# Kernel tuning notes

Hardware: AMD Instinct MI355X
Metric: run time of the kernel (lower is better)

The kernel has to match this reference:

```python
import jax, jax.numpy as jnp
import numpy as np

EPS = float(np.finfo(np.float32).eps)


def fake_quant_w(w):
    # per-output-channel symmetric int8 fake quant; w: (out, in)
    w_d = jax.lax.stop_gradient(w)
    max_abs = jnp.max(jnp.abs(w_d), axis=1, keepdims=True)
    scale = jnp.maximum(max_abs / 127.0, EPS)
    w_q = jnp.clip(jnp.round(w_d / scale), -127, 127)
    return w_q * scale


def woq_linear(x, w, b):
    return x @ fake_quant_w(w).T + b


def setup_inputs() -> dict:
    key = jax.random.key(0)
    ks = jax.random.split(key, 9)
    dim = 1024
    B, S = 2, 2048
    def wmat(k):
        return jax.random.normal(k, (dim, dim), dtype=jnp.float32) * (1.0 / np.sqrt(dim))
    def bvec(k):
        return jax.random.normal(k, (dim,), dtype=jnp.float32) * 0.01
    return {
        "x": jax.random.normal(ks[0], (B, S, dim), dtype=jnp.float32),
        "wq": wmat(ks[1]), "bq": bvec(ks[2]),
        "wk": wmat(ks[3]), "bk": bvec(ks[4]),
        "wv": wmat(ks[5]), "bv": bvec(ks[6]),
        "wp": wmat(ks[7]), "bp": bvec(ks[8]),
    }


def reference(x, wq, bq, wk, bk, wv, bv, wp, bp):
    B, S, C = x.shape
    H = 16
    D = C // H
    scale = D ** -0.5
    # QKV projections with fake-quantized weights -> (B, H, S, D)
    q = woq_linear(x, wq, bq).reshape(B, S, H, D).transpose(0, 2, 1, 3)
    k = woq_linear(x, wk, bk).reshape(B, S, H, D).transpose(0, 2, 1, 3)
    v = woq_linear(x, wv, bv).reshape(B, S, H, D).transpose(0, 2, 1, 3)
    attn = jnp.einsum("bhsd,bhtd->bhst", q, k) * scale  # (B,H,S,S)
    attn = jax.nn.softmax(attn, axis=-1)
    out = jnp.einsum("bhst,bhtd->bhsd", attn, v)
    out = out.transpose(0, 2, 1, 3).reshape(B, S, C)
    return woq_linear(out, wp, bp)
```

## Files before the change

### kernel.cpp

```cpp
#include <hip/hip_runtime.h>
#include <stdint.h>

typedef short bf16x8 __attribute__((ext_vector_type(8)));
typedef float f32x4 __attribute__((ext_vector_type(4)));
typedef uint16_t u16;
typedef uint32_t u32;
typedef u16 u16x4 __attribute__((ext_vector_type(4)));
typedef u32 u32x4 __attribute__((ext_vector_type(4)));

#define EPSF 1.1920929e-07f

static __device__ __forceinline__ u16 f2bf(float f) {
  union { float f; uint32_t u; } v; v.f = f;
  return (u16)((v.u + 0x7FFFu + ((v.u >> 16) & 1u)) >> 16);
}
static __device__ __forceinline__ float bf2f(u16 h) {
  union { uint32_t u; float f; } v; v.u = ((uint32_t)h) << 16;
  return v.f;
}
static __device__ __forceinline__ float exp2_fast(float x) {
  return __builtin_amdgcn_exp2f(x);
}
static __device__ __forceinline__ u32 cvt_pk_bf16(float lo, float hi) {
  u32 r;
  asm("v_cvt_pk_bf16_f32 %0, %1, %2" : "=v"(r) : "v"(lo), "v"(hi));
  return r;
}
static __device__ __forceinline__ void gload_lds16(const void* g, void* l) {
  __builtin_amdgcn_global_load_lds(
      (const __attribute__((address_space(1))) void*)g,
      (__attribute__((address_space(3))) void*)l, 16, 0, 0);
}
template <int N>
static __device__ __forceinline__ void vmwait() {
  asm volatile("s_waitcnt vmcnt(%0)" ::"i"(N) : "memory");
}

__global__ __launch_bounds__(256) void prep_kernel(
    const float* __restrict__ wq, const float* __restrict__ wk,
    const float* __restrict__ wv, const float* __restrict__ wp,
    const float* __restrict__ x,
    u16* __restrict__ wout, float* __restrict__ scales, u16* __restrict__ xb) {
  const int t = threadIdx.x;
  if (blockIdx.x < 4096) {
    const int row = blockIdx.x & 1023;
    const int mat = blockIdx.x >> 10;
    const float* W = (mat == 0) ? wq : (mat == 1) ? wk : (mat == 2) ? wv : wp;
    const float4 v = ((const float4*)(W + (size_t)row * 1024))[t];
    float m = fmaxf(fmaxf(fabsf(v.x), fabsf(v.y)), fmaxf(fabsf(v.z), fabsf(v.w)));
#pragma unroll
    for (int off = 1; off < 64; off <<= 1) m = fmaxf(m, __shfl_xor(m, off));
    __shared__ float red[4];
    if ((t & 63) == 0) red[t >> 6] = m;
    __syncthreads();
    m = fmaxf(fmaxf(red[0], red[1]), fmaxf(red[2], red[3]));
    const float scale = fmaxf(m / 127.0f, EPSF);
    float q0 = fminf(fmaxf(rintf(v.x / scale), -127.f), 127.f);
    float q1 = fminf(fmaxf(rintf(v.y / scale), -127.f), 127.f);
    float q2 = fminf(fmaxf(rintf(v.z / scale), -127.f), 127.f);
    float q3 = fminf(fmaxf(rintf(v.w / scale), -127.f), 127.f);
    u16x4 o; o.x = f2bf(q0); o.y = f2bf(q1); o.z = f2bf(q2); o.w = f2bf(q3);
    *(u16x4*)(wout + ((size_t)(mat * 1024 + row)) * 1024 + t * 4) = o;
    if (t == 0) scales[mat * 1024 + row] = scale;
  } else {
    const int i = (blockIdx.x - 4096) * 256 + t;
    const float4 v = ((const float4*)x)[i];
    u16x4 hv;
    hv.x = f2bf(v.x); hv.y = f2bf(v.y); hv.z = f2bf(v.z); hv.w = f2bf(v.w);
    *(u16x4*)(xb + (size_t)i * 4) = hv;
  }
}

template <int MODE, int MR, int NR, int NT, int KT, int LDA>
__global__ __launch_bounds__(512) void gemm_kernel(
    const u16* __restrict__ A, const u16* __restrict__ Bw,
    const float* __restrict__ scales, const float* __restrict__ b0,
    const float* __restrict__ b1, const float* __restrict__ b2,
    u16* __restrict__ qkv, float* __restrict__ outp) {
  constexpr int BM = 2 * MR * 16;
  constexpr int BN = 4 * NR * 16;
  constexpr int OPS = BM / 64 + BN / 64;
  __shared__ u16 As[2][BM * 64];
  __shared__ u16 Bs[2][BN * 64];
  const int tid = threadIdx.x;
  const int w = tid >> 6, l = tid & 63;
  const int per = gridDim.x >> 3;
  const int L = (blockIdx.x & 7) * per + (blockIdx.x >> 3);
  const int tile_n = (L % NT) * BN;
  const int tile_m = (L / NT) * BM;
  const int wm = w >> 2, wn = w & 3;
  const int l15 = l & 15, l4 = l >> 4;
  const int sw = l15 & 7;

  f32x4 acc[MR][NR];
  const f32x4 vzero = {0.f, 0.f, 0.f, 0.f};
#pragma unroll
  for (int m = 0; m < MR; ++m)
#pragma unroll
    for (int n = 0; n < NR; ++n) acc[m][n] = vzero;

  const int r8 = tid >> 3;
  const int g = tid & 7;
  const int gs = g ^ (r8 & 7);
  auto STAGE = [&](int slot, int j) {
    const int kb = j * 64;
    const int kbB = kb & 1023;
#pragma unroll
    for (int i = 0; i < BM / 64; ++i)
      gload_lds16(A + (size_t)(tile_m + i * 64 + r8) * LDA + kb + gs * 8,
                  &As[slot][(i * 64 + r8) * 64 + g * 8]);
#pragma unroll
    for (int i = 0; i < BN / 64; ++i)
      gload_lds16(Bw + (size_t)(tile_n + i * 64 + r8) * 1024 + kbB + gs * 8,
                  &Bs[slot][(i * 64 + r8) * 64 + g * 8]);
  };

  STAGE(0, 0);
  STAGE(1, 1);
  vmwait<OPS>();
  __builtin_amdgcn_s_barrier();

  for (int j = 0; j < KT; ++j) {
    const int cur = j & 1;
#pragma unroll
    for (int ks = 0; ks < 2; ++ks) {
      bf16x8 af[MR], bfv[NR];
      const int sg8 = ((ks * 4 + l4) ^ sw) * 8;
#pragma unroll
      for (int m = 0; m < MR; ++m)
        af[m] = *(const bf16x8*)(&As[cur][(wm * (MR * 16) + m * 16 + l15) * 64 + sg8]);
#pragma unroll
      for (int n = 0; n < NR; ++n)
        bfv[n] = *(const bf16x8*)(&Bs[cur][(wn * (NR * 16) + n * 16 + l15) * 64 + sg8]);
      __builtin_amdgcn_s_setprio(1);
#pragma unroll
      for (int m = 0; m < MR; ++m)
#pragma unroll
        for (int n = 0; n < NR; ++n)
          acc[m][n] = __builtin_amdgcn_mfma_f32_16x16x32_bf16(af[m], bfv[n], acc[m][n], 0, 0, 0);
      __builtin_amdgcn_s_setprio(0);
    }
    __builtin_amdgcn_s_barrier();
    if (j + 2 < KT) {
      STAGE(cur, j + 2);
      vmwait<OPS>();
    } else {
      vmwait<0>();
    }
    __builtin_amdgcn_s_barrier();
  }

#pragma unroll
  for (int m = 0; m < MR; ++m) {
#pragma unroll
    for (int n = 0; n < NR; ++n) {
      const int col = tile_n + wn * (NR * 16) + n * 16 + l15;
      const float sc = scales[col];
      if constexpr (MODE == 0) {
        const int mat = col >> 10, oo = col & 1023;
        const float* bias = (mat == 0) ? b0 : (mat == 1) ? b1 : b2;
        const float bb = bias[oo];
        const int hh = oo >> 6, dd = oo & 63;
        if (mat == 2) {
          const int rowm0 = tile_m + wm * (MR * 16) + m * 16 + l4 * 4;
          const int b = rowm0 >> 11, s = rowm0 & 2047;
          u16x4 pk;
#pragma unroll
          for (int jj = 0; jj < 4; ++jj) pk[jj] = f2bf(acc[m][n][jj] * sc + bb);
          const int kpos = (s & ~31) + ((s >> 2) & 3) * 8 + ((s >> 4) & 1) * 4;
          *(u16x4*)(qkv + (size_t)2 * 4194304 +
                    ((size_t)(b * 16 + hh) * 64 + dd) * 2048 + kpos) = pk;
        } else {
#pragma unroll
          for (int jj = 0; jj < 4; ++jj) {
            const int rowm = tile_m + wm * (MR * 16) + m * 16 + l4 * 4 + jj;
            const int b = rowm >> 11, s = rowm & 2047;
            float y = acc[m][n][jj] * sc + bb;
            if (mat == 0) y *= 0.18033688011112042f;
            qkv[(size_t)mat * 4194304 + ((size_t)(b * 16 + hh) * 2048 + s) * 64 + dd] = f2bf(y);
          }
        }
      } else {
        const float bb = b0[col];
#pragma unroll
        for (int jj = 0; jj < 4; ++jj) {
          const int rowm = tile_m + wm * (MR * 16) + m * 16 + l4 * 4 + jj;
          outp[(size_t)rowm * 1024 + col] = acc[m][n][jj] * sc + bb;
        }
      }
    }
  }
}

__global__ __launch_bounds__(512, 4) void attn_kernel(
    const u16* __restrict__ qg, const u16* __restrict__ kg,
    const u16* __restrict__ vtg, u16* __restrict__ po) {
  __shared__ u16 Kt[2][2][64 * 64];
  __shared__ u16 Vt[2][2][64 * 64];
  const int tid = threadIdx.x;
  const int w = tid >> 6, l = tid & 63;
  const int Lb = (blockIdx.x & 7) * 64 + (blockIdx.x >> 3);
  const int bh = Lb >> 4;
  const int qt = Lb & 15;
  const u16* qp = qg + (size_t)bh * 131072;
  const u16* kp = kg + (size_t)bh * 131072;
  const u16* vp = vtg + (size_t)bh * 131072;
  const int wg = w & 3, grp = w >> 2;
  const int qrow0 = qt * 128 + wg * 32;
  const int l15 = l & 15, l4 = l >> 4;
  const int sw = l15 & 7;

  const int sr = tid >> 3, sg = tid & 7;
  const int gsw = (sg ^ (sr & 7)) << 3;
  auto STAGE = [&](const int slot, const int j) {
    const int kA = j * 64, kB = 1024 + j * 64;
    gload_lds16(kp + (size_t)(kA + sr) * 64 + gsw, &Kt[slot][0][tid * 8]);
    gload_lds16(vp + (size_t)sr * 2048 + kA + gsw, &Vt[slot][0][tid * 8]);
    gload_lds16(kp + (size_t)(kB + sr) * 64 + gsw, &Kt[slot][1][tid * 8]);
    gload_lds16(vp + (size_t)sr * 2048 + kB + gsw, &Vt[slot][1][tid * 8]);
  };

  bf16x8 qfr[2][2];
#pragma unroll
  for (int dk = 0; dk < 2; ++dk)
#pragma unroll
    for (int qf = 0; qf < 2; ++qf)
      qfr[dk][qf] =
          *(const bf16x8*)(qp + (size_t)(qrow0 + qf * 16 + l15) * 64 + dk * 32 + l4 * 8);

  const f32x4 vzero = {0.f, 0.f, 0.f, 0.f};
  f32x4 O[4][2];
#pragma unroll
  for (int di = 0; di < 4; ++di)
#pragma unroll
    for (int qf = 0; qf < 2; ++qf) O[di][qf] = vzero;
  float lrun[2] = {0.f, 0.f};

  auto DO_ITER = [&](const int slot, const int j) {
    const u16* Kb = &Kt[slot][grp][0];
    const u16* Vb = &Vt[slot][grp][0];

    f32x4 sfr[2][4];
#pragma unroll
    for (int qf = 0; qf < 2; ++qf)
#pragma unroll
      for (int ki = 0; ki < 4; ++ki) sfr[qf][ki] = vzero;
#pragma unroll
    for (int dk = 0; dk < 2; ++dk) {
      bf16x8 kf[4];
#pragma unroll
      for (int ki = 0; ki < 4; ++ki)
        kf[ki] = *(const bf16x8*)(Kb + (ki * 16 + l15) * 64 + (((dk * 4 + l4) ^ sw) << 3));
      __builtin_amdgcn_s_setprio(1);
#pragma unroll
      for (int ki = 0; ki < 4; ++ki)
#pragma unroll
        for (int qf = 0; qf < 2; ++qf)
          sfr[qf][ki] = __builtin_amdgcn_mfma_f32_16x16x32_bf16(kf[ki], qfr[dk][qf], sfr[qf][ki], 0, 0, 0);
      __builtin_amdgcn_s_setprio(0);
    }

    u32 pw[2][8];
#pragma unroll
    for (int qf = 0; qf < 2; ++qf) {
      float rs = 0.f;
#pragma unroll
      for (int ki = 0; ki < 4; ++ki) {
        const f32x4 s4 = sfr[qf][ki];
        const float p0 = exp2_fast(s4[0]);
        const float p1 = exp2_fast(s4[1]);
        const float p2 = exp2_fast(s4[2]);
        const float p3 = exp2_fast(s4[3]);
        rs += (p0 + p1) + (p2 + p3);
        pw[qf][ki * 2 + 0] = cvt_pk_bf16(p0, p1);
        pw[qf][ki * 2 + 1] = cvt_pk_bf16(p2, p3);
      }
      lrun[qf] += rs;
    }

#pragma unroll
    for (int kkl = 0; kkl < 2; ++kkl) {
      const u32x4 t0 = {pw[0][kkl * 4 + 0], pw[0][kkl * 4 + 1],
                        pw[0][kkl * 4 + 2], pw[0][kkl * 4 + 3]};
      const u32x4 t1 = {pw[1][kkl * 4 + 0], pw[1][kkl * 4 + 1],
                        pw[1][kkl * 4 + 2], pw[1][kkl * 4 + 3]};
      const bf16x8 pf0 = __builtin_bit_cast(bf16x8, t0);
      const bf16x8 pf1 = __builtin_bit_cast(bf16x8, t1);
      bf16x8 vf[4];
#pragma unroll
      for (int di = 0; di < 4; ++di)
        vf[di] = *(const bf16x8*)(Vb + (di * 16 + l15) * 64 +
                                  (((kkl * 4 + l4) ^ sw) << 3));
      __builtin_amdgcn_s_setprio(1);
#pragma unroll
      for (int di = 0; di < 4; ++di) {
        O[di][0] = __builtin_amdgcn_mfma_f32_16x16x32_bf16(pf0, vf[di], O[di][0], 0, 0, 0);
        O[di][1] = __builtin_amdgcn_mfma_f32_16x16x32_bf16(pf1, vf[di], O[di][1], 0, 0, 0);
      }
      __builtin_amdgcn_s_setprio(0);
    }

    __builtin_amdgcn_s_barrier();
    if (j + 2 < 16) {
      STAGE(slot, j + 2);
      vmwait<4>();
    } else {
      vmwait<0>();
    }
    __builtin_amdgcn_s_barrier();
  };

  STAGE(0, 0);
  STAGE(1, 1);
  vmwait<4>();
  __builtin_amdgcn_s_barrier();

  for (int jp = 0; jp < 8; ++jp) {
    DO_ITER(0, jp * 2);
    DO_ITER(1, jp * 2 + 1);
  }

  float* Osh = (float*)&Kt[0][0][0];
  float* lsh = (float*)&Vt[0][0][0];
  if (grp == 1) {
    float* ob = Osh + (0 * 4 + wg) * 1024;
#pragma unroll
    for (int di = 0; di < 4; ++di)
#pragma unroll
      for (int jj = 0; jj < 4; ++jj)
        ob[(l4 * 4 + jj) * 64 + di * 16 + l15] = O[di][0][jj];
    lsh[(0 * 4 + wg) * 64 + l] = lrun[0];
  } else {
    float* ob = Osh + (1 * 4 + wg) * 1024;
#pragma unroll
    for (int di = 0; di < 4; ++di)
#pragma unroll
      for (int jj = 0; jj < 4; ++jj)
        ob[(l4 * 4 + jj) * 64 + di * 16 + l15] = O[di][1][jj];
    lsh[(1 * 4 + wg) * 64 + l] = lrun[1];
  }
  __syncthreads();
  const int b = bh >> 4, hh = bh & 15;
  if (grp == 0) {
    const float* obr = Osh + (0 * 4 + wg) * 1024;
    float lt = lrun[0] + lsh[(0 * 4 + wg) * 64 + l];
    lt += __shfl_xor(lt, 16);
    lt += __shfl_xor(lt, 32);
    float lq[4];
#pragma unroll
    for (int jj = 0; jj < 4; ++jj)
      lq[jj] = __builtin_amdgcn_rcpf(__shfl(lt, l4 * 4 + jj));
#pragma unroll
    for (int di = 0; di < 4; ++di)
#pragma unroll
      for (int jj = 0; jj < 4; ++jj) {
        const float oval =
            (O[di][0][jj] + obr[(l4 * 4 + jj) * 64 + di * 16 + l15]) * lq[jj];
        const int srw = qrow0 + l4 * 4 + jj;
        const int c = hh * 64 + di * 16 + l15;
        po[((size_t)(b * 2048 + srw)) * 1024 + c] = f2bf(oval);
      }
  } else {
    const float* obr = Osh + (1 * 4 + wg) * 1024;
    float lt = lrun[1] + lsh[(1 * 4 + wg) * 64 + l];
    lt += __shfl_xor(lt, 16);
    lt += __shfl_xor(lt, 32);
    float lq[4];
#pragma unroll
    for (int jj = 0; jj < 4; ++jj)
      lq[jj] = __builtin_amdgcn_rcpf(__shfl(lt, l4 * 4 + jj));
#pragma unroll
    for (int di = 0; di < 4; ++di)
#pragma unroll
      for (int jj = 0; jj < 4; ++jj) {
        const float oval =
            (O[di][1][jj] + obr[(l4 * 4 + jj) * 64 + di * 16 + l15]) * lq[jj];
        const int srw = qrow0 + 16 + l4 * 4 + jj;
        const int c = hh * 64 + di * 16 + l15;
        po[((size_t)(b * 2048 + srw)) * 1024 + c] = f2bf(oval);
      }
  }
}

extern "C" void kernel_launch(void* const* d_in, const int* in_sizes, int n_in,
                              void* d_out, int out_size, void* d_ws, size_t ws_size,
                              hipStream_t stream) {
  (void)in_sizes; (void)n_in; (void)out_size; (void)ws_size;
  const float* x  = (const float*)d_in[0];
  const float* wq = (const float*)d_in[1];
  const float* bq = (const float*)d_in[2];
  const float* wk = (const float*)d_in[3];
  const float* bk = (const float*)d_in[4];
  const float* wv = (const float*)d_in[5];
  const float* bv = (const float*)d_in[6];
  const float* wp = (const float*)d_in[7];
  const float* bp = (const float*)d_in[8];

  char* ws = (char*)d_ws;
  u16*   wquant = (u16*)ws;
  float* scales = (float*)(ws + 8388608);
  u16*   xb     = (u16*)(ws + 8404992);
  u16*   po     = xb;
  u16*   qkv    = (u16*)(ws + 25182208);

  prep_kernel<<<dim3(8192), dim3(256), 0, stream>>>(
      wq, wk, wv, wp, x, wquant, scales, xb);
  gemm_kernel<0, 4, 3, 16, 16, 1024><<<dim3(512), dim3(512), 0, stream>>>(
      xb, wquant, scales, bq, bk, bv, qkv, nullptr);
  attn_kernel<<<dim3(512), dim3(512), 0, stream>>>(
      qkv, qkv + 4194304, qkv + 8388608, po);
  gemm_kernel<1, 2, 2, 8, 16, 1024><<<dim3(512), dim3(512), 0, stream>>>(
      po, wquant + 3145728, scales + 3072, bp, nullptr, nullptr, nullptr, (float*)d_out);
}
```

Baseline: 96.38 us.

## Halve attention block threads and give each wave 64 query rows

The attention kernel now runs 4 waves per block instead of 8, and each wave handles 64 query rows (4 MFMA fragments) instead of 32. Each K/V fragment read from LDS is therefore reused across twice as many query rows, which cuts LDS read traffic per MFMA. Staging is split into two loads per thread, and the split-K merge epilogue is reworked to match. The cost is higher register pressure from the larger accumulator and score arrays, fewer waves to hide latency, and launch bounds lowered to (256,2).

```diff
diff --git a/kernel.cpp b/kernel.cpp
--- a/kernel.cpp
+++ b/kernel.cpp
@@ -192,7 +192,7 @@
   }
 }
 
-__global__ __launch_bounds__(512, 4) void attn_kernel(
+__global__ __launch_bounds__(256, 2) void attn_kernel(
     const u16* __restrict__ qg, const u16* __restrict__ kg,
     const u16* __restrict__ vtg, u16* __restrict__ po) {
   __shared__ u16 Kt[2][2][64 * 64];
@@ -205,44 +205,48 @@
   const u16* qp = qg + (size_t)bh * 131072;
   const u16* kp = kg + (size_t)bh * 131072;
   const u16* vp = vtg + (size_t)bh * 131072;
-  const int wg = w & 3, grp = w >> 2;
-  const int qrow0 = qt * 128 + wg * 32;
+  const int wg = w & 1, grp = w >> 1;
+  const int qrow0 = qt * 128 + wg * 64;
   const int l15 = l & 15, l4 = l >> 4;
   const int sw = l15 & 7;
 
-  const int sr = tid >> 3, sg = tid & 7;
-  const int gsw = (sg ^ (sr & 7)) << 3;
   auto STAGE = [&](const int slot, const int j) {
     const int kA = j * 64, kB = 1024 + j * 64;
-    gload_lds16(kp + (size_t)(kA + sr) * 64 + gsw, &Kt[slot][0][tid * 8]);
-    gload_lds16(vp + (size_t)sr * 2048 + kA + gsw, &Vt[slot][0][tid * 8]);
-    gload_lds16(kp + (size_t)(kB + sr) * 64 + gsw, &Kt[slot][1][tid * 8]);
-    gload_lds16(vp + (size_t)sr * 2048 + kB + gsw, &Vt[slot][1][tid * 8]);
+#pragma unroll
+    for (int i = 0; i < 2; ++i) {
+      const int c = i * 256 + tid;
+      const int r = c >> 3, g = c & 7;
+      const int gg = (g ^ (r & 7)) << 3;
+      gload_lds16(kp + (size_t)(kA + r) * 64 + gg, &Kt[slot][0][c * 8]);
+      gload_lds16(vp + (size_t)r * 2048 + kA + gg, &Vt[slot][0][c * 8]);
+      gload_lds16(kp + (size_t)(kB + r) * 64 + gg, &Kt[slot][1][c * 8]);
+      gload_lds16(vp + (size_t)r * 2048 + kB + gg, &Vt[slot][1][c * 8]);
+    }
   };
 
-  bf16x8 qfr[2][2];
+  bf16x8 qfr[2][4];
 #pragma unroll
   for (int dk = 0; dk < 2; ++dk)
 #pragma unroll
-    for (int qf = 0; qf < 2; ++qf)
+    for (int qf = 0; qf < 4; ++qf)
       qfr[dk][qf] =
           *(const bf16x8*)(qp + (size_t)(qrow0 + qf * 16 + l15) * 64 + dk * 32 + l4 * 8);
 
   const f32x4 vzero = {0.f, 0.f, 0.f, 0.f};
-  f32x4 O[4][2];
+  f32x4 O[4][4];
 #pragma unroll
   for (int di = 0; di < 4; ++di)
 #pragma unroll
-    for (int qf = 0; qf < 2; ++qf) O[di][qf] = vzero;
-  float lrun[2] = {0.f, 0.f};
+    for (int qf = 0; qf < 4; ++qf) O[di][qf] = vzero;
+  float lrun[4] = {0.f, 0.f, 0.f, 0.f};
 
   auto DO_ITER = [&](const int slot, const int j) {
     const u16* Kb = &Kt[slot][grp][0];
     const u16* Vb = &Vt[slot][grp][0];
 
-    f32x4 sfr[2][4];
-#pragma unroll
-    for (int qf = 0; qf < 2; ++qf)
+    f32x4 sfr[4][4];
+#pragma unroll
+    for (int qf = 0; qf < 4; ++qf)
 #pragma unroll
       for (int ki = 0; ki < 4; ++ki) sfr[qf][ki] = vzero;
 #pragma unroll
@@ -255,14 +259,14 @@
 #pragma unroll
       for (int ki = 0; ki < 4; ++ki)
 #pragma unroll
-        for (int qf = 0; qf < 2; ++qf)
+        for (int qf = 0; qf < 4; ++qf)
           sfr[qf][ki] = __builtin_amdgcn_mfma_f32_16x16x32_bf16(kf[ki], qfr[dk][qf], sfr[qf][ki], 0, 0, 0);
       __builtin_amdgcn_s_setprio(0);
     }
 
-    u32 pw[2][8];
-#pragma unroll
-    for (int qf = 0; qf < 2; ++qf) {
+    u32 pw[4][8];
+#pragma unroll
+    for (int qf = 0; qf < 4; ++qf) {
       float rs = 0.f;
 #pragma unroll
       for (int ki = 0; ki < 4; ++ki) {
@@ -280,12 +284,13 @@
 
 #pragma unroll
     for (int kkl = 0; kkl < 2; ++kkl) {
-      const u32x4 t0 = {pw[0][kkl * 4 + 0], pw[0][kkl * 4 + 1],
-                        pw[0][kkl * 4 + 2], pw[0][kkl * 4 + 3]};
-      const u32x4 t1 = {pw[1][kkl * 4 + 0], pw[1][kkl * 4 + 1],
-                        pw[1][kkl * 4 + 2], pw[1][kkl * 4 + 3]};
-      const bf16x8 pf0 = __builtin_bit_cast(bf16x8, t0);
-      const bf16x8 pf1 = __builtin_bit_cast(bf16x8, t1);
+      bf16x8 pf[4];
+#pragma unroll
+      for (int qf = 0; qf < 4; ++qf) {
+        const u32x4 t = {pw[qf][kkl * 4 + 0], pw[qf][kkl * 4 + 1],
+                         pw[qf][kkl * 4 + 2], pw[qf][kkl * 4 + 3]};
+        pf[qf] = __builtin_bit_cast(bf16x8, t);
+      }
       bf16x8 vf[4];
 #pragma unroll
       for (int di = 0; di < 4; ++di)
@@ -293,17 +298,17 @@
                                   (((kkl * 4 + l4) ^ sw) << 3));
       __builtin_amdgcn_s_setprio(1);
 #pragma unroll
-      for (int di = 0; di < 4; ++di) {
-        O[di][0] = __builtin_amdgcn_mfma_f32_16x16x32_bf16(pf0, vf[di], O[di][0], 0, 0, 0);
-        O[di][1] = __builtin_amdgcn_mfma_f32_16x16x32_bf16(pf1, vf[di], O[di][1], 0, 0, 0);
-      }
+      for (int di = 0; di < 4; ++di)
+#pragma unroll
+        for (int qf = 0; qf < 4; ++qf)
+          O[di][qf] = __builtin_amdgcn_mfma_f32_16x16x32_bf16(pf[qf], vf[di], O[di][qf], 0, 0, 0);
       __builtin_amdgcn_s_setprio(0);
     }
 
     __builtin_amdgcn_s_barrier();
     if (j + 2 < 16) {
       STAGE(slot, j + 2);
-      vmwait<4>();
+      vmwait<8>();
     } else {
       vmwait<0>();
     }
@@ -312,7 +317,7 @@
 
   STAGE(0, 0);
   STAGE(1, 1);
-  vmwait<4>();
+  vmwait<8>();
   __builtin_amdgcn_s_barrier();
 
   for (int jp = 0; jp < 8; ++jp) {
@@ -322,63 +327,75 @@
 
   float* Osh = (float*)&Kt[0][0][0];
   float* lsh = (float*)&Vt[0][0][0];
-  if (grp == 1) {
-    float* ob = Osh + (0 * 4 + wg) * 1024;
-#pragma unroll
-    for (int di = 0; di < 4; ++di)
-#pragma unroll
-      for (int jj = 0; jj < 4; ++jj)
-        ob[(l4 * 4 + jj) * 64 + di * 16 + l15] = O[di][0][jj];
-    lsh[(0 * 4 + wg) * 64 + l] = lrun[0];
+  if (grp == 0) {
+#pragma unroll
+    for (int qq = 0; qq < 2; ++qq) {
+      float* ob = Osh + (wg * 2 + qq) * 1024;
+#pragma unroll
+      for (int di = 0; di < 4; ++di)
+#pragma unroll
+        for (int jj = 0; jj < 4; ++jj)
+          ob[(l4 * 4 + jj) * 64 + di * 16 + l15] = O[di][2 + qq][jj];
+      lsh[(wg * 2 + qq) * 64 + l] = lrun[2 + qq];
+    }
   } else {
-    float* ob = Osh + (1 * 4 + wg) * 1024;
-#pragma unroll
-    for (int di = 0; di < 4; ++di)
-#pragma unroll
-      for (int jj = 0; jj < 4; ++jj)
-        ob[(l4 * 4 + jj) * 64 + di * 16 + l15] = O[di][1][jj];
-    lsh[(1 * 4 + wg) * 64 + l] = lrun[1];
+#pragma unroll
+    for (int qq = 0; qq < 2; ++qq) {
+      float* ob = Osh + (4 + wg * 2 + qq) * 1024;
+#pragma unroll
+      for (int di = 0; di < 4; ++di)
+#pragma unroll
+        for (int jj = 0; jj < 4; ++jj)
+          ob[(l4 * 4 + jj) * 64 + di * 16 + l15] = O[di][qq][jj];
+      lsh[(4 + wg * 2 + qq) * 64 + l] = lrun[qq];
+    }
   }
   __syncthreads();
   const int b = bh >> 4, hh = bh & 15;
   if (grp == 0) {
-    const float* obr = Osh + (0 * 4 + wg) * 1024;
-    float lt = lrun[0] + lsh[(0 * 4 + wg) * 64 + l];
-    lt += __shfl_xor(lt, 16);
-    lt += __shfl_xor(lt, 32);
-    float lq[4];
-#pragma unroll
-    for (int jj = 0; jj < 4; ++jj)
-      lq[jj] = __builtin_amdgcn_rcpf(__shfl(lt, l4 * 4 + jj));
-#pragma unroll
-    for (int di = 0; di < 4; ++di)
-#pragma unroll
-      for (int jj = 0; jj < 4; ++jj) {
-        const float oval =
-            (O[di][0][jj] + obr[(l4 * 4 + jj) * 64 + di * 16 + l15]) * lq[jj];
-        const int srw = qrow0 + l4 * 4 + jj;
-        const int c = hh * 64 + di * 16 + l15;
-        po[((size_t)(b * 2048 + srw)) * 1024 + c] = f2bf(oval);
-      }
+#pragma unroll
+    for (int qq = 0; qq < 2; ++qq) {
+      const float* obr = Osh + (4 + wg * 2 + qq) * 1024;
+      float lt = lrun[qq] + lsh[(4 + wg * 2 + qq) * 64 + l];
+      lt += __shfl_xor(lt, 16);
+      lt += __shfl_xor(lt, 32);
+      float lq[4];
+#pragma unroll
+      for (int jj = 0; jj < 4; ++jj)
+        lq[jj] = __builtin_amdgcn_rcpf(__shfl(lt, l4 * 4 + jj));
+#pragma unroll
+      for (int di = 0; di < 4; ++di)
+#pragma unroll
+        for (int jj = 0; jj < 4; ++jj) {
+          const float oval =
+              (O[di][qq][jj] + obr[(l4 * 4 + jj) * 64 + di * 16 + l15]) * lq[jj];
+          const int srw = qrow0 + qq * 16 + l4 * 4 + jj;
+          const int c = hh * 64 + di * 16 + l15;
+          po[((size_t)(b * 2048 + srw)) * 1024 + c] = f2bf(oval);
+        }
+    }
   } else {
-    const float* obr = Osh + (1 * 4 + wg) * 1024;
-    float lt = lrun[1] + lsh[(1 * 4 + wg) * 64 + l];
-    lt += __shfl_xor(lt, 16);
-    lt += __shfl_xor(lt, 32);
-    float lq[4];
-#pragma unroll
-    for (int jj = 0; jj < 4; ++jj)
-      lq[jj] = __builtin_amdgcn_rcpf(__shfl(lt, l4 * 4 + jj));
-#pragma unroll
-    for (int di = 0; di < 4; ++di)
-#pragma unroll
-      for (int jj = 0; jj < 4; ++jj) {
-        const float oval =
-            (O[di][1][jj] + obr[(l4 * 4 + jj) * 64 + di * 16 + l15]) * lq[jj];
-        const int srw = qrow0 + 16 + l4 * 4 + jj;
-        const int c = hh * 64 + di * 16 + l15;
-        po[((size_t)(b * 2048 + srw)) * 1024 + c] = f2bf(oval);
-      }
+#pragma unroll
+    for (int qq = 0; qq < 2; ++qq) {
+      const float* obr = Osh + (wg * 2 + qq) * 1024;
+      float lt = lrun[2 + qq] + lsh[(wg * 2 + qq) * 64 + l];
+      lt += __shfl_xor(lt, 16);
+      lt += __shfl_xor(lt, 32);
+      float lq[4];
+#pragma unroll
+      for (int jj = 0; jj < 4; ++jj)
+        lq[jj] = __builtin_amdgcn_rcpf(__shfl(lt, l4 * 4 + jj));
+#pragma unroll
+      for (int di = 0; di < 4; ++di)
+#pragma unroll
+        for (int jj = 0; jj < 4; ++jj) {
+          const float oval =
+              (O[di][2 + qq][jj] + obr[(l4 * 4 + jj) * 64 + di * 16 + l15]) * lq[jj];
+          const int srw = qrow0 + (2 + qq) * 16 + l4 * 4 + jj;
+          const int c = hh * 64 + di * 16 + l15;
+          po[((size_t)(b * 2048 + srw)) * 1024 + c] = f2bf(oval);
+        }
+    }
   }
 }
 
@@ -407,7 +424,7 @@
       wq, wk, wv, wp, x, wquant, scales, xb);
   gemm_kernel<0, 4, 3, 16, 16, 1024><<<dim3(512), dim3(512), 0, stream>>>(
       xb, wquant, scales, bq, bk, bv, qkv, nullptr);
-  attn_kernel<<<dim3(512), dim3(512), 0, stream>>>(
+  attn_kernel<<<dim3(512), dim3(256), 0, stream>>>(
       qkv, qkv + 4194304, qkv + 8388608, po);
   gemm_kernel<1, 2, 2, 8, 16, 1024><<<dim3(512), dim3(512), 0, stream>>>(
       po, wquant + 3145728, scales + 3072, bp, nullptr, nullptr, nullptr, (float*)d_out);
```

Measured after the change: 117.0 us. +21.4%, slower.
